# Kernel tuning notes

Hardware: AMD Instinct MI355X
Metric: run time of the kernel (lower is better)

Reference implementation:

```python
import jax, jax.numpy as jnp
import numpy as np

B, S, D, H = 2, 2048, 1024, 16
HD = D // H  # head_dim = 64


def _rope(t, cos, sin):
    # t: (B, H, S, HD); cos/sin: (S, HD//2) -> rotate interleaved pairs
    t2 = t.reshape(*t.shape[:-1], HD // 2, 2)
    t1, t2_ = t2[..., 0], t2[..., 1]
    c = cos[None, None, :, :]
    s = sin[None, None, :, :]
    out = jnp.stack([t1 * c - t2_ * s, t1 * s + t2_ * c], axis=-1)
    return out.reshape(t.shape)


def setup_inputs() -> dict:
    key = jax.random.key(0)
    ks = jax.random.split(key, 5)
    x = jax.random.normal(ks[0], (B, S, D), dtype=jnp.float32)
    attn_mask = jnp.tril(jnp.ones((S, S), dtype=bool))  # causal
    # standard RoPE angles: pos * inv_freq
    inv_freq = 1.0 / (10000.0 ** (jnp.arange(0, HD, 2, dtype=jnp.float32) / HD))
    freqs = jnp.arange(S, dtype=jnp.float32)[:, None] * inv_freq[None, :]  # (S, HD//2)
    std = 1.0 / np.sqrt(D)
    w_qkv = jax.random.normal(ks[1], (3 * D, D), dtype=jnp.float32) * std
    b_qkv = jnp.zeros((3 * D,), dtype=jnp.float32)
    w_proj = jax.random.normal(ks[2], (D, D), dtype=jnp.float32) * std
    b_proj = jnp.zeros((D,), dtype=jnp.float32)
    return {"x": x, "attn_mask": attn_mask, "freqs": freqs,
            "w_qkv": w_qkv, "b_qkv": b_qkv, "w_proj": w_proj, "b_proj": b_proj}


def reference(x, attn_mask, freqs, w_qkv, b_qkv, w_proj, b_proj):
    # QKV projection: (B,S,D) -> (B,S,3D), split per einops pattern (three, H, HD)
    qkv = x @ w_qkv.T + b_qkv
    qkv = qkv.reshape(B, S, 3, H, HD)
    q = jnp.transpose(qkv[:, :, 0], (0, 2, 1, 3))  # (B,H,S,HD)
    k = jnp.transpose(qkv[:, :, 1], (0, 2, 1, 3))
    v = jnp.transpose(qkv[:, :, 2], (0, 2, 1, 3))
    cos, sin = jnp.cos(freqs), jnp.sin(freqs)
    q = _rope(q, cos, sin)
    k = _rope(k, cos, sin)
    scale = 1.0 / np.sqrt(HD)
    scores = jnp.einsum("bhqd,bhkd->bhqk", q, k) * scale  # (B,H,S,S)
    scores = jnp.where(attn_mask[None, None, :, :], scores, jnp.finfo(scores.dtype).min)
    attn = jax.nn.softmax(scores, axis=-1)
    out = jnp.einsum("bhqk,bhkd->bhqd", attn, v)  # (B,H,S,HD)
    out = jnp.transpose(out, (0, 2, 1, 3)).reshape(B, S, D)
    return out @ w_proj.T + b_proj
```

## Files before the change

### kernel.cpp

```cpp
#include <hip/hip_runtime.h>

#define S_LEN 2048
#define NH 16
#define HD 64
#define DMODEL 1024

typedef __bf16 bf16x8 __attribute__((ext_vector_type(8)));
typedef float floatx4 __attribute__((ext_vector_type(4)));
typedef short short8 __attribute__((ext_vector_type(8)));

__device__ inline unsigned short f2bf(float f) {
    union { float f; unsigned u; } v; v.f = f;
    unsigned u = v.u;
    unsigned r = (u + 0x7FFFu + ((u >> 16) & 1u)) >> 16;
    return (unsigned short)r;
}

__device__ __forceinline__ void gload_lds16(const void* g, void* l) {
    __builtin_amdgcn_global_load_lds(
        (const __attribute__((address_space(1))) unsigned int*)g,
        (__attribute__((address_space(3))) unsigned int*)l, 16, 0, 0);
}

#define WAITV_BAR(N) do { \
    asm volatile("s_waitcnt vmcnt(" #N ")\n\ts_barrier" ::: "memory"); \
    __builtin_amdgcn_sched_barrier(0); \
} while (0)

__device__ __forceinline__ void cvt4(const float4* __restrict__ src,
                                     uint2* __restrict__ dst, int i) {
    float4 v = src[i];
    union { unsigned short u[4]; uint2 d; } o;
    o.u[0] = f2bf(v.x); o.u[1] = f2bf(v.y); o.u[2] = f2bf(v.z); o.u[3] = f2bf(v.w);
    dst[i] = o.d;
}

__global__ __launch_bounds__(256) void prep_kernel(
    const float* __restrict__ x, const float* __restrict__ wq,
    const float* __restrict__ wp, const float* __restrict__ freqs,
    unsigned short* __restrict__ xb, unsigned short* __restrict__ wqb,
    unsigned short* __restrict__ wpb, float2* __restrict__ cs)
{
    const int tid = blockIdx.x * 256 + threadIdx.x;
    const int nth = gridDim.x * 256;
    for (int i = tid; i < (4096 * 1024) / 4; i += nth) cvt4((const float4*)x, (uint2*)xb, i);
    for (int i = tid; i < (3072 * 1024) / 4; i += nth) cvt4((const float4*)wq, (uint2*)wqb, i);
    for (int i = tid; i < (1024 * 1024) / 4; i += nth) cvt4((const float4*)wp, (uint2*)wpb, i);
    for (int i = tid; i < S_LEN * 32; i += nth) {
        const float f = freqs[i];
        float2 c; c.x = cosf(f); c.y = sinf(f);
        cs[i] = c;
    }
}

#define SROW(r) (((r) & 3) ^ (((r) >> 2) & 3))

#define QKV_STAGE(bi, kk) do { \
    unsigned short* dA_ = smem + (bi) * 8192; \
    unsigned short* dB_ = dA_ + 4096; \
    gload_lds16(ag + (kk),               dA_ + wv * 512); \
    gload_lds16(ag + 64 * DMODEL + (kk), dA_ + 2048 + wv * 512); \
    gload_lds16(bg + (kk),               dB_ + wv * 512); \
    gload_lds16(bg + 64 * DMODEL + (kk), dB_ + 2048 + wv * 512); \
} while (0)

#define QKV_COMPUTE(bi) do { \
    const unsigned short* sA_ = smem + (bi) * 8192; \
    const unsigned short* sB_ = sA_ + 4096; \
    bf16x8 af[4]; \
    _Pragma("unroll") for (int m_ = 0; m_ < 4; m_++) af[m_] = *(const bf16x8*)&sA_[aoff[m_]]; \
    _Pragma("unroll") for (int n_ = 0; n_ < 4; n_++) { \
        bf16x8 bf = *(const bf16x8*)&sB_[boff[n_]]; \
        _Pragma("unroll") for (int m_ = 0; m_ < 4; m_++) \
            acc[m_][n_] = __builtin_amdgcn_mfma_f32_16x16x32_bf16(af[m_], bf, acc[m_][n_], 0, 0, 0); \
    } \
} while (0)

__global__ __launch_bounds__(256, 3) void qkv_gemm_kernel(
    const unsigned short* __restrict__ xb, const unsigned short* __restrict__ wqb,
    const float* __restrict__ bias, const float2* __restrict__ cs,
    unsigned short* __restrict__ qb, unsigned short* __restrict__ kb,
    unsigned short* __restrict__ vb)
{
    __shared__ __align__(16) unsigned short smem[24576];

    const int t = threadIdx.x;
    const int v = (blockIdx.x & 7) * 96 + (blockIdx.x >> 3);
    const int mbase = (v / 24) * 128;
    const int nbase = (v % 24) * 128;
    const int wv = t >> 6, lane = t & 63;
    const int quad = lane >> 4, l16 = lane & 15;
    const int wr = wv >> 1, wc = wv & 1;

    floatx4 acc[4][4];
    #pragma unroll
    for (int m = 0; m < 4; m++)
        #pragma unroll
        for (int n = 0; n < 4; n++)
            #pragma unroll
            for (int r = 0; r < 4; r++) acc[m][n][r] = 0.f;

    const int srow = t >> 2;
    const int schunk = (t & 3) ^ SROW(srow);
    const unsigned short* ag = xb + (size_t)(mbase + srow) * DMODEL + schunk * 8;
    const unsigned short* bg = wqb + (size_t)(nbase + srow) * DMODEL + schunk * 8;

    const int Sl = SROW(l16);
    int aoff[4], boff[4];
    #pragma unroll
    for (int m = 0; m < 4; m++) aoff[m] = (wr * 64 + m * 16 + l16) * 32 + (quad ^ Sl) * 8;
    #pragma unroll
    for (int n = 0; n < 4; n++) boff[n] = (wc * 64 + n * 16 + l16) * 32 + (quad ^ Sl) * 8;

    QKV_STAGE(0, 0);
    QKV_STAGE(1, 32);
    for (int tb = 0; tb < 30; tb += 3) {
        WAITV_BAR(4); QKV_STAGE(2, (tb + 2) * 32); QKV_COMPUTE(0);
        WAITV_BAR(4); QKV_STAGE(0, (tb + 3) * 32); QKV_COMPUTE(1);
        WAITV_BAR(4); QKV_STAGE(1, (tb + 4) * 32); QKV_COMPUTE(2);
    }
    WAITV_BAR(4); QKV_COMPUTE(0);
    WAITV_BAR(0); QKV_COMPUTE(1);

    const int part = nbase >> 10;
    const int bidx = mbase >> 11;
    const int s0   = mbase & 2047;

    if (part == 2) {
        unsigned short* Vt = smem;
        const int hb = (nbase & 1023) >> 6;
        float bvv[4];
        #pragma unroll
        for (int nt = 0; nt < 4; nt++) bvv[nt] = bias[nbase + wc * 64 + nt * 16 + l16];
        #pragma unroll
        for (int shalf = 0; shalf < 2; shalf++) {
            __syncthreads();
            if (wr == shalf) {
                #pragma unroll
                for (int nt = 0; nt < 4; nt++) {
                    const int hdl = wc * 64 + nt * 16 + l16;
                    #pragma unroll
                    for (int m = 0; m < 4; m++)
                        #pragma unroll
                        for (int r = 0; r < 4; r++)
                            Vt[hdl * 72 + m * 16 + quad * 4 + r] = f2bf(acc[m][nt][r] + bvv[nt]);
                }
            }
            __syncthreads();
            const int hdl = t & 127, sp = t >> 7;
            const size_t bh2 = (size_t)bidx * NH + hb + (hdl >> 6);
            #pragma unroll
            for (int c = 0; c < 4; c++) {
                const int sl0 = (sp * 4 + c) * 8;
                const int sg = s0 + shalf * 64 + sl0;
                short8 vv = *(const short8*)&Vt[hdl * 72 + sl0];
                *(short8*)&vb[((bh2 * 256 + (sg >> 3)) * 64 + (hdl & 63)) * 8] = vv;
            }
        }
    } else {
        const size_t bhb = (size_t)bidx * NH;
        const int odd = l16 & 1;
        #pragma unroll
        for (int nt = 0; nt < 4; nt++) {
            const int n_ = nbase + wc * 64 + nt * 16 + l16;
            const int hd = n_ & 63;
            const size_t bh = bhb + ((n_ & 1023) >> 6);
            const float bvv = bias[n_];
            const int ci = (nt * 16 + l16) >> 1;
            #pragma unroll
            for (int m = 0; m < 4; m++) {
                #pragma unroll
                for (int r = 0; r < 4; r++) {
                    const int s = s0 + wr * 64 + m * 16 + quad * 4 + r;
                    float val = acc[m][nt][r] + bvv;
                    float other = __shfl_xor(val, 1, 64);
                    const float2 csv = cs[(size_t)s * 32 + ci];
                    float outv = odd ? fmaf(other, csv.y, val * csv.x)
                                     : fmaf(-other, csv.y, val * csv.x);
                    if (part == 0) {
                        qb[(bh * S_LEN + s) * HD + hd] = f2bf(outv * 0.125f);
                    } else {
                        kb[((bh * 8 + (hd >> 3)) * (size_t)S_LEN + s) * 8 + (hd & 7)] = f2bf(outv);
                    }
                }
            }
        }
    }
}

__global__ __launch_bounds__(256, 3) void attn_kernel(
    const unsigned short* __restrict__ qb, const unsigned short* __restrict__ kb,
    const unsigned short* __restrict__ vbk, unsigned short* __restrict__ ao)
{
    __shared__ __align__(16) unsigned short Ks[2][8 * 512];
    __shared__ __align__(16) unsigned short Vt[2][8 * 512];
    __shared__ __align__(16) unsigned short Pw[4][16 * 72];

    const int t = threadIdx.x;
    const int wv = t >> 6, lane = t & 63, quad = lane >> 4, l16 = lane & 15;
    const int qt   = 31 - (blockIdx.x >> 5);
    const int bhid = blockIdx.x & 31;
    const int h = bhid & 15, b = bhid >> 4;
    const size_t bh = (size_t)b * NH + h;
    const unsigned short* qg  = qb + bh * S_LEN * HD;
    const unsigned short* kgB = kb + bh * 8 * S_LEN * 8;
    const unsigned short* vgB = vbk + bh * 256 * 64 * 8;

    bf16x8 qf[2];
    {
        const unsigned short* q0 = qg + (size_t)(qt * 64 + wv * 16 + l16) * HD;
        qf[0] = *(const bf16x8*)&q0[quad * 8];
        qf[1] = *(const bf16x8*)&q0[32 + quad * 8];
    }

    bf16x8 ones;
    {
        union { short8 s; bf16x8 v; } o;
        for (int j = 0; j < 8; j++) o.s[j] = 0x3F80;
        ones = o.v;
    }

    floatx4 lfr = {0.f, 0.f, 0.f, 0.f};
    floatx4 Ofr[4];
    for (int nt = 0; nt < 4; nt++)
        for (int r = 0; r < 4; r++) Ofr[nt][r] = 0.f;

    const int ntiles = qt + 1;

#define ATTN_STAGE(bufi, kt_) do { \
    const int kb_ = (kt_) * 64; \
    const unsigned short* g0 = kgB + ((size_t)(2 * wv) * S_LEN + kb_ + lane) * 8; \
    gload_lds16(g0,             &Ks[bufi][(2 * wv) * 512]); \
    gload_lds16(g0 + S_LEN * 8, &Ks[bufi][(2 * wv + 1) * 512]); \
    const unsigned short* g1 = vgB + ((size_t)((kb_ >> 3) + 2 * wv) * 64 + lane) * 8; \
    gload_lds16(g1,          &Vt[bufi][(2 * wv) * 512]); \
    gload_lds16(g1 + 64 * 8, &Vt[bufi][(2 * wv + 1) * 512]); \
} while (0)

#define ATTN_COMPUTE(bufi, kt_) do { \
    const int kbase = (kt_) * 64; \
    float pex[4][4]; \
    _Pragma("unroll") for (int sub = 0; sub < 4; sub++) { \
        bf16x8 kf0 = *(const bf16x8*)&Ks[bufi][(0 * 4 + quad) * 512 + (sub * 16 + l16) * 8]; \
        bf16x8 kf1 = *(const bf16x8*)&Ks[bufi][(1 * 4 + quad) * 512 + (sub * 16 + l16) * 8]; \
        floatx4 sacc = {0.f, 0.f, 0.f, 0.f}; \
        sacc = __builtin_amdgcn_mfma_f32_16x16x32_bf16(kf0, qf[0], sacc, 0, 0, 0); \
        sacc = __builtin_amdgcn_mfma_f32_16x16x32_bf16(kf1, qf[1], sacc, 0, 0, 0); \
        _Pragma("unroll") for (int r = 0; r < 4; r++) pex[sub][r] = sacc[r]; \
    } \
    if ((kt_) == qt) { \
        const int q = qt * 64 + wv * 16 + l16; \
        _Pragma("unroll") for (int sub = 0; sub < 4; sub++) \
            _Pragma("unroll") for (int r = 0; r < 4; r++) { \
                const int key = kbase + sub * 16 + quad * 4 + r; \
                if (key > q) pex[sub][r] = -1e30f; \
            } \
    } \
    _Pragma("unroll") for (int sub = 0; sub < 4; sub++) { \
        union { unsigned short s[4]; uint2 u; } pk; \
        _Pragma("unroll") for (int r = 0; r < 4; r++) pk.s[r] = f2bf(__expf(pex[sub][r])); \
        *(uint2*)&Pw[wv][l16 * 72 + sub * 16 + quad * 4] = pk.u; \
    } \
    { \
        bf16x8 pf0 = *(const bf16x8*)&Pw[wv][l16 * 72 + quad * 8]; \
        bf16x8 pf1 = *(const bf16x8*)&Pw[wv][l16 * 72 + 32 + quad * 8]; \
        lfr = __builtin_amdgcn_mfma_f32_16x16x32_bf16(ones, pf0, lfr, 0, 0, 0); \
        lfr = __builtin_amdgcn_mfma_f32_16x16x32_bf16(ones, pf1, lfr, 0, 0, 0); \
        _Pragma("unroll") for (int nt = 0; nt < 4; nt++) { \
            bf16x8 v0 = *(const bf16x8*)&Vt[bufi][(0 * 4 + quad) * 512 + (nt * 16 + l16) * 8]; \
            bf16x8 v1 = *(const bf16x8*)&Vt[bufi][(1 * 4 + quad) * 512 + (nt * 16 + l16) * 8]; \
            Ofr[nt] = __builtin_amdgcn_mfma_f32_16x16x32_bf16(pf0, v0, Ofr[nt], 0, 0, 0); \
            Ofr[nt] = __builtin_amdgcn_mfma_f32_16x16x32_bf16(pf1, v1, Ofr[nt], 0, 0, 0); \
        } \
    } \
} while (0)

    ATTN_STAGE(0, 0);
    __syncthreads();
    for (int kt = 0; kt < ntiles; ) {
        if (kt + 1 < ntiles) ATTN_STAGE(1, kt + 1);
        ATTN_COMPUTE(0, kt);
        kt++;
        if (kt >= ntiles) break;
        __syncthreads();
        if (kt + 1 < ntiles) ATTN_STAGE(0, kt + 1);
        ATTN_COMPUTE(1, kt);
        kt++;
        if (kt >= ntiles) break;
        __syncthreads();
    }

    float linv[4];
    #pragma unroll
    for (int r = 0; r < 4; r++) {
        float lq = __shfl(lfr[0], (lane & 48) | (quad * 4 + r), 64);
        linv[r] = 1.f / lq;
    }
    #pragma unroll
    for (int nt = 0; nt < 4; nt++)
        #pragma unroll
        for (int r = 0; r < 4; r++) {
            const int s = qt * 64 + wv * 16 + quad * 4 + r;
            ao[((size_t)b * S_LEN + s) * DMODEL + h * HD + nt * 16 + l16] =
                f2bf(Ofr[nt][r] * linv[r]);
        }
#undef ATTN_STAGE
#undef ATTN_COMPUTE
}

#define PROJ_STAGE(bi, kk) do { \
    unsigned short* dA_ = smem + (bi) * 6144; \
    unsigned short* dB_ = dA_ + 4096; \
    gload_lds16(ag + (kk),               dA_ + wv * 512); \
    gload_lds16(ag + 64 * DMODEL + (kk), dA_ + 2048 + wv * 512); \
    gload_lds16(bg + (kk),               dB_ + wv * 512); \
} while (0)

#define PROJ_COMPUTE(bi) do { \
    const unsigned short* sA_ = smem + (bi) * 6144; \
    const unsigned short* sB_ = sA_ + 4096; \
    bf16x8 af[4]; \
    _Pragma("unroll") for (int m_ = 0; m_ < 4; m_++) af[m_] = *(const bf16x8*)&sA_[aoff[m_]]; \
    _Pragma("unroll") for (int n_ = 0; n_ < 2; n_++) { \
        bf16x8 bf = *(const bf16x8*)&sB_[boff[n_]]; \
        _Pragma("unroll") for (int m_ = 0; m_ < 4; m_++) \
            acc[m_][n_] = __builtin_amdgcn_mfma_f32_16x16x32_bf16(af[m_], bf, acc[m_][n_], 0, 0, 0); \
    } \
} while (0)

__global__ __launch_bounds__(256, 3) void proj_kernel(
    const unsigned short* __restrict__ a, const unsigned short* __restrict__ wpb,
    const float* __restrict__ bias, float* __restrict__ out)
{
    __shared__ __align__(16) unsigned short smem[18432];

    const int t = threadIdx.x;
    const int v = (blockIdx.x & 7) * 64 + (blockIdx.x >> 3);
    const int mbase = (v >> 4) * 128;
    const int nbase = (v & 15) * 64;
    const int wv = t >> 6, lane = t & 63, quad = lane >> 4, l16 = lane & 15;
    const int wr = wv >> 1, wc = wv & 1;

    floatx4 acc[4][2];
    #pragma unroll
    for (int m = 0; m < 4; m++)
        #pragma unroll
        for (int n = 0; n < 2; n++)
            #pragma unroll
            for (int r = 0; r < 4; r++) acc[m][n][r] = 0.f;

    const int srow = t >> 2;
    const int schunk = (t & 3) ^ SROW(srow);
    const unsigned short* ag = a + (size_t)(mbase + srow) * DMODEL + schunk * 8;
    const unsigned short* bg = wpb + (size_t)(nbase + srow) * DMODEL + schunk * 8;

    const int Sl = SROW(l16);
    int aoff[4], boff[2];
    #pragma unroll
    for (int m = 0; m < 4; m++) aoff[m] = (wr * 64 + m * 16 + l16) * 32 + (quad ^ Sl) * 8;
    #pragma unroll
    for (int n = 0; n < 2; n++) boff[n] = (wc * 32 + n * 16 + l16) * 32 + (quad ^ Sl) * 8;

    PROJ_STAGE(0, 0);
    PROJ_STAGE(1, 32);
    for (int tb = 0; tb < 30; tb += 3) {
        WAITV_BAR(3); PROJ_STAGE(2, (tb + 2) * 32); PROJ_COMPUTE(0);
        WAITV_BAR(3); PROJ_STAGE(0, (tb + 3) * 32); PROJ_COMPUTE(1);
        WAITV_BAR(3); PROJ_STAGE(1, (tb + 4) * 32); PROJ_COMPUTE(2);
    }
    WAITV_BAR(3); PROJ_COMPUTE(0);
    WAITV_BAR(0); PROJ_COMPUTE(1);

    #pragma unroll
    for (int n = 0; n < 2; n++) {
        const int nn = nbase + wc * 32 + n * 16 + l16;
        const float bvv = bias[nn];
        #pragma unroll
        for (int m = 0; m < 4; m++)
            #pragma unroll
            for (int r = 0; r < 4; r++)
                out[(size_t)(mbase + wr * 64 + m * 16 + quad * 4 + r) * DMODEL + nn] =
                    acc[m][n][r] + bvv;
    }
}

extern "C" void kernel_launch(void* const* d_in, const int* in_sizes, int n_in,
                              void* d_out, int out_size, void* d_ws, size_t ws_size,
                              hipStream_t stream) {
    const float* x      = (const float*)d_in[0];
    const float* freqs  = (const float*)d_in[2];
    const float* w_qkv  = (const float*)d_in[3];
    const float* b_qkv  = (const float*)d_in[4];
    const float* w_proj = (const float*)d_in[5];
    const float* b_proj = (const float*)d_in[6];
    float* out = (float*)d_out;

    unsigned short* ws = (unsigned short*)d_ws;
    const size_t HSZ = (size_t)2 * NH * S_LEN * HD;
    unsigned short* qb  = ws;
    unsigned short* kb  = ws + HSZ;
    unsigned short* vb  = ws + 2 * HSZ;
    unsigned short* ao  = ws + 3 * HSZ;
    unsigned short* xb  = ws + 4 * HSZ;
    unsigned short* wqb = xb + (size_t)4096 * 1024;
    unsigned short* wpb = wqb + (size_t)3072 * 1024;
    float2* cs = (float2*)(wpb + (size_t)1024 * 1024);

    prep_kernel<<<2048, 256, 0, stream>>>(x, w_qkv, w_proj, freqs, xb, wqb, wpb, cs);
    qkv_gemm_kernel<<<768, 256, 0, stream>>>(xb, wqb, b_qkv, cs, qb, kb, vb);
    attn_kernel<<<1024, 256, 0, stream>>>(qb, kb, vb, ao);
    proj_kernel<<<512, 256, 0, stream>>>(ao, wpb, b_proj, out);
}
```

Baseline: 195.5 us.

## Enlarge QKV GEMM tile to 256x128 with 512 threads; add setprio around attention MFMAs

The QKV projection GEMM now uses 512-thread blocks computing 256x128 output tiles, with a new XCD-aware block-to-tile mapping, three-stage LDS buffers sized for the larger A tile, and a V-transpose epilogue that walks four 64-row chunks. The larger tile reuses each loaded B (weight) tile across twice as many rows, cutting global and L2 traffic, while the mapping groups tiles per XCD for L2 locality. Separately, the attention kernel wraps its MFMA sections in s_setprio to favor matrix work while other waves issue loads. Risks include lower occupancy from the larger shared memory footprint and the 512-thread launch bound, and only 384 blocks to fill the device.

Result: slower. 215.5 us (+10.3%).

```diff
diff --git a/kernel.cpp b/kernel.cpp
--- a/kernel.cpp
+++ b/kernel.cpp
@@ -56,17 +56,15 @@
 #define SROW(r) (((r) & 3) ^ (((r) >> 2) & 3))
 
 #define QKV_STAGE(bi, kk) do { \
-    unsigned short* dA_ = smem + (bi) * 8192; \
-    unsigned short* dB_ = dA_ + 4096; \
-    gload_lds16(ag + (kk),               dA_ + wv * 512); \
-    gload_lds16(ag + 64 * DMODEL + (kk), dA_ + 2048 + wv * 512); \
-    gload_lds16(bg + (kk),               dB_ + wv * 512); \
-    gload_lds16(bg + 64 * DMODEL + (kk), dB_ + 2048 + wv * 512); \
+    unsigned short* S_ = smem + (bi) * 12288; \
+    gload_lds16(agp0 + (kk), S_ + wv * 1024); \
+    gload_lds16(agp1 + (kk), S_ + wv * 1024 + 512); \
+    gload_lds16(bgp  + (kk), S_ + 8192 + wv * 512); \
 } while (0)
 
 #define QKV_COMPUTE(bi) do { \
-    const unsigned short* sA_ = smem + (bi) * 8192; \
-    const unsigned short* sB_ = sA_ + 4096; \
+    const unsigned short* sA_ = smem + (bi) * 12288; \
+    const unsigned short* sB_ = sA_ + 8192; \
     bf16x8 af[4]; \
     _Pragma("unroll") for (int m_ = 0; m_ < 4; m_++) af[m_] = *(const bf16x8*)&sA_[aoff[m_]]; \
     _Pragma("unroll") for (int n_ = 0; n_ < 4; n_++) { \
@@ -76,18 +74,18 @@
     } \
 } while (0)
 
-__global__ __launch_bounds__(256, 3) void qkv_gemm_kernel(
+__global__ __launch_bounds__(512, 4) void qkv_gemm_kernel(
     const unsigned short* __restrict__ xb, const unsigned short* __restrict__ wqb,
     const float* __restrict__ bias, const float2* __restrict__ cs,
     unsigned short* __restrict__ qb, unsigned short* __restrict__ kb,
     unsigned short* __restrict__ vb)
 {
-    __shared__ __align__(16) unsigned short smem[24576];
+    __shared__ __align__(16) unsigned short smem[36864];
 
     const int t = threadIdx.x;
-    const int v = (blockIdx.x & 7) * 96 + (blockIdx.x >> 3);
-    const int mbase = (v / 24) * 128;
-    const int nbase = (v % 24) * 128;
+    const int xcd = blockIdx.x & 7, rr = blockIdx.x >> 3;
+    const int mbase = ((xcd & 3) * 4 + rr / 12) * 256;
+    const int nbase = ((xcd >> 2) * 12 + rr % 12) * 128;
     const int wv = t >> 6, lane = t & 63;
     const int quad = lane >> 4, l16 = lane & 15;
     const int wr = wv >> 1, wc = wv & 1;
@@ -100,10 +98,13 @@
             #pragma unroll
             for (int r = 0; r < 4; r++) acc[m][n][r] = 0.f;
 
-    const int srow = t >> 2;
-    const int schunk = (t & 3) ^ SROW(srow);
-    const unsigned short* ag = xb + (size_t)(mbase + srow) * DMODEL + schunk * 8;
-    const unsigned short* bg = wqb + (size_t)(nbase + srow) * DMODEL + schunk * 8;
+    const int lA0 = wv * 128 + lane, lA1 = lA0 + 64, lB = wv * 64 + lane;
+    const int arow0 = lA0 >> 2, achk0 = (lA0 & 3) ^ SROW(arow0);
+    const int arow1 = lA1 >> 2, achk1 = (lA1 & 3) ^ SROW(arow1);
+    const int brow  = lB >> 2,  bchk  = (lB & 3) ^ SROW(brow);
+    const unsigned short* agp0 = xb + (size_t)(mbase + arow0) * DMODEL + achk0 * 8;
+    const unsigned short* agp1 = xb + (size_t)(mbase + arow1) * DMODEL + achk1 * 8;
+    const unsigned short* bgp  = wqb + (size_t)(nbase + brow) * DMODEL + bchk * 8;
 
     const int Sl = SROW(l16);
     int aoff[4], boff[4];
@@ -115,11 +116,11 @@
     QKV_STAGE(0, 0);
     QKV_STAGE(1, 32);
     for (int tb = 0; tb < 30; tb += 3) {
-        WAITV_BAR(4); QKV_STAGE(2, (tb + 2) * 32); QKV_COMPUTE(0);
-        WAITV_BAR(4); QKV_STAGE(0, (tb + 3) * 32); QKV_COMPUTE(1);
-        WAITV_BAR(4); QKV_STAGE(1, (tb + 4) * 32); QKV_COMPUTE(2);
-    }
-    WAITV_BAR(4); QKV_COMPUTE(0);
+        WAITV_BAR(3); QKV_STAGE(2, (tb + 2) * 32); QKV_COMPUTE(0);
+        WAITV_BAR(3); QKV_STAGE(0, (tb + 3) * 32); QKV_COMPUTE(1);
+        WAITV_BAR(3); QKV_STAGE(1, (tb + 4) * 32); QKV_COMPUTE(2);
+    }
+    WAITV_BAR(3); QKV_COMPUTE(0);
     WAITV_BAR(0); QKV_COMPUTE(1);
 
     const int part = nbase >> 10;
@@ -133,9 +134,9 @@
         #pragma unroll
         for (int nt = 0; nt < 4; nt++) bvv[nt] = bias[nbase + wc * 64 + nt * 16 + l16];
         #pragma unroll
-        for (int shalf = 0; shalf < 2; shalf++) {
+        for (int chunk = 0; chunk < 4; chunk++) {
             __syncthreads();
-            if (wr == shalf) {
+            if (wr == chunk) {
                 #pragma unroll
                 for (int nt = 0; nt < 4; nt++) {
                     const int hdl = wc * 64 + nt * 16 + l16;
@@ -150,9 +151,9 @@
             const int hdl = t & 127, sp = t >> 7;
             const size_t bh2 = (size_t)bidx * NH + hb + (hdl >> 6);
             #pragma unroll
-            for (int c = 0; c < 4; c++) {
-                const int sl0 = (sp * 4 + c) * 8;
-                const int sg = s0 + shalf * 64 + sl0;
+            for (int c = 0; c < 2; c++) {
+                const int sl0 = sp * 16 + c * 8;
+                const int sg = s0 + chunk * 64 + sl0;
                 short8 vv = *(const short8*)&Vt[hdl * 72 + sl0];
                 *(short8*)&vb[((bh2 * 256 + (sg >> 3)) * 64 + (hdl & 63)) * 8] = vv;
             }
@@ -240,6 +241,7 @@
 #define ATTN_COMPUTE(bufi, kt_) do { \
     const int kbase = (kt_) * 64; \
     float pex[4][4]; \
+    __builtin_amdgcn_s_setprio(1); \
     _Pragma("unroll") for (int sub = 0; sub < 4; sub++) { \
         bf16x8 kf0 = *(const bf16x8*)&Ks[bufi][(0 * 4 + quad) * 512 + (sub * 16 + l16) * 8]; \
         bf16x8 kf1 = *(const bf16x8*)&Ks[bufi][(1 * 4 + quad) * 512 + (sub * 16 + l16) * 8]; \
@@ -248,6 +250,7 @@
         sacc = __builtin_amdgcn_mfma_f32_16x16x32_bf16(kf1, qf[1], sacc, 0, 0, 0); \
         _Pragma("unroll") for (int r = 0; r < 4; r++) pex[sub][r] = sacc[r]; \
     } \
+    __builtin_amdgcn_s_setprio(0); \
     if ((kt_) == qt) { \
         const int q = qt * 64 + wv * 16 + l16; \
         _Pragma("unroll") for (int sub = 0; sub < 4; sub++) \
@@ -264,6 +267,7 @@
     { \
         bf16x8 pf0 = *(const bf16x8*)&Pw[wv][l16 * 72 + quad * 8]; \
         bf16x8 pf1 = *(const bf16x8*)&Pw[wv][l16 * 72 + 32 + quad * 8]; \
+        __builtin_amdgcn_s_setprio(1); \
         lfr = __builtin_amdgcn_mfma_f32_16x16x32_bf16(ones, pf0, lfr, 0, 0, 0); \
         lfr = __builtin_amdgcn_mfma_f32_16x16x32_bf16(ones, pf1, lfr, 0, 0, 0); \
         _Pragma("unroll") for (int nt = 0; nt < 4; nt++) { \
@@ -272,6 +276,7 @@
             Ofr[nt] = __builtin_amdgcn_mfma_f32_16x16x32_bf16(pf0, v0, Ofr[nt], 0, 0, 0); \
             Ofr[nt] = __builtin_amdgcn_mfma_f32_16x16x32_bf16(pf1, v1, Ofr[nt], 0, 0, 0); \
         } \
+        __builtin_amdgcn_s_setprio(0); \
     } \
 } while (0)
 
@@ -407,7 +412,7 @@
     float2* cs = (float2*)(wpb + (size_t)1024 * 1024);
 
     prep_kernel<<<2048, 256, 0, stream>>>(x, w_qkv, w_proj, freqs, xb, wqb, wpb, cs);
-    qkv_gemm_kernel<<<768, 256, 0, stream>>>(xb, wqb, b_qkv, cs, qb, kb, vb);
+    qkv_gemm_kernel<<<384, 512, 0, stream>>>(xb, wqb, b_qkv, cs, qb, kb, vb);
     attn_kernel<<<1024, 256, 0, stream>>>(qb, kb, vb, ao);
     proj_kernel<<<512, 256, 0, stream>>>(ao, wpb, b_proj, out);
 }
```
